# Optimization experiments

Hardware: AMD Instinct MI355X
Metric: run time of the kernel (lower is better)

The kernel has to match this reference:

```python
import jax, jax.numpy as jnp
import numpy as np

B, N, E, D, H, K = 64, 2048, 512, 256, 256, 5
I = E + D  # GRU input dim


def setup_inputs() -> dict:
    key = jax.random.key(0)
    ks = jax.random.split(key, 12)
    s = 0.05  # weight init scale
    enc_z = jax.random.normal(ks[0], (B, N, E), jnp.float32)
    dec_z = jax.random.normal(ks[1], (B, D), jnp.float32)
    h0 = jax.random.normal(ks[2], (1, B, H), jnp.float32)
    # GRU params (torch layout: gates ordered r, z, n)
    W_ih = jax.random.normal(ks[3], (3 * H, I), jnp.float32) * s
    W_hh = jax.random.normal(ks[4], (3 * H, H), jnp.float32) * s
    b_ih = jax.random.normal(ks[5], (3 * H,), jnp.float32) * s
    b_hh = jax.random.normal(ks[6], (3 * H,), jnp.float32) * s
    # K per-component MLPs: Linear(H,H) -> tanh -> Linear(H,3), stacked over K
    W1 = jax.random.normal(ks[7], (K, H, H), jnp.float32) * s
    b1 = jax.random.normal(ks[8], (K, H), jnp.float32) * s
    W2 = jax.random.normal(ks[9], (K, 3, H), jnp.float32) * s
    b2 = jax.random.normal(ks[10], (K, 3), jnp.float32) * s
    return {"enc_z": enc_z, "dec_z": dec_z, "h0": h0,
            "W_ih": W_ih, "W_hh": W_hh, "b_ih": b_ih, "b_hh": b_hh,
            "W1": W1, "b1": b1, "W2": W2, "b2": b2, "i": 0}


def reference(enc_z, dec_z, h0, W_ih, W_hh, b_ih, b_hh, W1, b1, W2, b2, i):
    # i == 0 -> reset: c = zeros, means = zeros, h = h0 (provided)
    Bt, Nt, Et = enc_z.shape
    Ht = h0.shape[-1]
    Kt = W1.shape[0]
    c0 = jnp.zeros((Bt, Et), enc_z.dtype)
    means = jnp.zeros((Bt, Kt), enc_z.dtype)
    # --- single-step GRU (torch semantics, gate order r,z,n) ---
    x = jnp.concatenate([dec_z, c0], axis=1)          # (B, I)
    h_prev = h0[0]                                    # (B, H)
    gi = x @ W_ih.T + b_ih                            # (B, 3H)
    gh = h_prev @ W_hh.T + b_hh                       # (B, 3H)
    r = jax.nn.sigmoid(gi[:, :Ht] + gh[:, :Ht])
    z = jax.nn.sigmoid(gi[:, Ht:2 * Ht] + gh[:, Ht:2 * Ht])
    n = jnp.tanh(gi[:, 2 * Ht:] + r * gh[:, 2 * Ht:])
    h_new = (1.0 - z) * n + z * h_prev                # (B, H)
    # --- K per-component MLPs, vectorized over K ---
    hid = jnp.tanh(jnp.einsum('khd,bd->bkh', W1, h_new) + b1)  # (B, K, H)
    params = jnp.einsum('kph,bkh->bkp', W2, hid) + b2           # (B, K, 3)
    # NOTE: the original code overwrites mean/scale each loop iteration, so
    # only the LAST component's mean/scale survive into the CDF loop.
    mean = means[:, Kt - 1] + jnp.exp(params[:, Kt - 1, 0])     # (B,)
    scale = jnp.exp(params[:, Kt - 1, 1])                       # (B,)
    weights = jax.nn.softmax(params[:, :, 2], axis=1)           # (B, K)
    # --- mixture-of-logistics CDF differences, vectorized over (B, N) ---
    # original _logistic: sigmoid(x - mean/scale)  (faithful to source, incl. its precedence)
    j = jnp.arange(Nt, dtype=enc_z.dtype)                       # (N,)
    arg = (mean / scale)[:, None]                               # (B, 1)
    f1 = jax.nn.sigmoid(j[None, :] + 0.5 - arg)                 # (B, N)
    f2 = jax.nn.sigmoid(j[None, :] - 0.5 - arg)                 # (B, N)
    # sum_k weights[:,k]*(f1-f2) with k-independent f1,f2 == weights.sum(1)*(f1-f2)
    a = weights.sum(axis=1, keepdims=True) * (f1 - f2)          # (B, N)
    c = jnp.einsum('bn,bne->be', a, enc_z)                      # (B, E)
    return (c[None], h_new[None])
```

## Files before the change

kernel.cpp:

```cpp
#include <hip/hip_runtime.h>
#include <hip/hip_bf16.h>
#include <cstdint>
#include <cstddef>

constexpr int B = 64, N = 2048, E = 512, D = 256, H = 256, K = 5, I = 768;

__device__ __forceinline__ float sg(float x) { return 1.0f / (1.0f + __expf(-x)); }

__device__ __forceinline__ void dot4(float4 v, const float* s, float& acc) {
  acc += v.x * s[0];
  acc += v.y * s[1];
  acc += v.z * s[2];
  acc += v.w * s[3];
}

__global__ __launch_bounds__(256) void fused(
    const float* __restrict__ enc, const float* __restrict__ dec,
    const float* __restrict__ h0,
    const float* __restrict__ Wih, const float* __restrict__ Whh,
    const float* __restrict__ bih, const float* __restrict__ bhh,
    const float* __restrict__ W1,  const float* __restrict__ b1,
    const float* __restrict__ W2,  const float* __restrict__ b2,
    float* __restrict__ out_c, float* __restrict__ out_h)
{
  __shared__ float xs[D], hs[H], hn[H], hid[K][H], pr[16];
  __shared__ float s_arg;
  const int b = blockIdx.x, t = threadIdx.x;
  xs[t] = dec[b * D + t];
  hs[t] = h0[b * H + t];
  __syncthreads();

  float gir = bih[t], giz = bih[H + t], gin = bih[2*H + t];
  float ghr = bhh[t], ghz = bhh[H + t], ghn = bhh[2*H + t];
  const float4* wr = reinterpret_cast<const float4*>(Wih + (size_t)t         * I);
  const float4* wz = reinterpret_cast<const float4*>(Wih + (size_t)(H + t)   * I);
  const float4* wn = reinterpret_cast<const float4*>(Wih + (size_t)(2*H + t) * I);
  const float4* ur = reinterpret_cast<const float4*>(Whh + (size_t)t         * H);
  const float4* uz = reinterpret_cast<const float4*>(Whh + (size_t)(H + t)   * H);
  const float4* un = reinterpret_cast<const float4*>(Whh + (size_t)(2*H + t) * H);
#pragma unroll 8
  for (int c = 0; c < 64; ++c) {
    dot4(wr[c], &xs[c*4], gir);
    dot4(wz[c], &xs[c*4], giz);
    dot4(wn[c], &xs[c*4], gin);
    dot4(ur[c], &hs[c*4], ghr);
    dot4(uz[c], &hs[c*4], ghz);
    dot4(un[c], &hs[c*4], ghn);
  }
  const float r = sg(gir + ghr);
  const float z = sg(giz + ghz);
  const float nn = tanhf(gin + r * ghn);
  const float hnew = (1.0f - z) * nn + z * hs[t];
  hn[t] = hnew;
  out_h[b * H + t] = hnew;
  __syncthreads();

#pragma unroll
  for (int k = 0; k < K; ++k) {
    float acc = b1[k * H + t];
    const float4* w = reinterpret_cast<const float4*>(W1 + ((size_t)k * H + t) * H);
#pragma unroll 8
    for (int c = 0; c < 64; ++c) dot4(w[c], &hn[c*4], acc);
    hid[k][t] = tanhf(acc);
  }
  __syncthreads();

  if (t < 240) {
    const int g = t >> 4, sub = t & 15;
    const int k = g / 3, p = g % 3;
    float s = 0.0f;
#pragma unroll
    for (int c = 0; c < 16; ++c) {
      const int h = sub + 16 * c;
      s += hid[k][h] * W2[(k * 3 + p) * H + h];
    }
    s += __shfl_xor(s, 8, 16);
    s += __shfl_xor(s, 4, 16);
    s += __shfl_xor(s, 2, 16);
    s += __shfl_xor(s, 1, 16);
    if (sub == 0) pr[g] = s + b2[k * 3 + p];
  }
  __syncthreads();

  if (t == 0) s_arg = __expf(pr[3 * (K - 1)] - pr[3 * (K - 1) + 1]);
  __syncthreads();

  const float arg = s_arg;
  const float lim = ceilf(arg) + 32.0f;
  int nmax = (lim < (float)N) ? (int)lim : N;
  if (nmax < 1) nmax = 1;

  const float2* src = reinterpret_cast<const float2*>(enc + (size_t)b * N * E) + t;
  float a0 = 0.0f, a1 = 0.0f;
#pragma unroll 4
  for (int n = 0; n < nmax; ++n) {
    const float fn = (float)n;
    const float an = sg(fn + 0.5f - arg) - sg(fn - 0.5f - arg);
    const float2 v = src[(size_t)n * (E / 2)];
    a0 += an * v.x;
    a1 += an * v.y;
  }
  out_c[b * E + 2 * t]     = a0;
  out_c[b * E + 2 * t + 1] = a1;
}

extern "C" void kernel_launch(void* const* d_in, const int* in_sizes, int n_in,
                              void* d_out, int out_size, void* d_ws, size_t ws_size,
                              hipStream_t stream) {
  const float* enc = (const float*)d_in[0];
  const float* dec = (const float*)d_in[1];
  const float* h0  = (const float*)d_in[2];
  const float* Wih = (const float*)d_in[3];
  const float* Whh = (const float*)d_in[4];
  const float* bih = (const float*)d_in[5];
  const float* bhh = (const float*)d_in[6];
  const float* W1  = (const float*)d_in[7];
  const float* b1  = (const float*)d_in[8];
  const float* W2  = (const float*)d_in[9];
  const float* b2  = (const float*)d_in[10];
  (void)in_sizes; (void)n_in; (void)out_size; (void)d_ws; (void)ws_size;

  float* out_c = (float*)d_out;
  float* out_h = out_c + (size_t)B * E;

  hipLaunchKernelGGL(fused, dim3(B), dim3(256), 0, stream,
                     enc, dec, h0, Wih, Whh, bih, bhh, W1, b1, W2, b2,
                     out_c, out_h);
}
```

Before: 404.9 us.

## Double block size and split GRU and MLP matvecs across thread halves

Launches 512 threads per batch block instead of 256. One half computes the input-gate matvec and the other the hidden-gate matvec, combining them through shared memory. The W1 matvec is also split by input halves with partial sums reduced in shared memory. The enc reduction now gives each thread one column instead of two. This shortens the per-thread serial dot-product chains in a kernel with only 64 blocks, at the cost of extra shared memory and syncs.

```diff
diff --git a/kernel.cpp b/kernel.cpp
--- a/kernel.cpp
+++ b/kernel.cpp
@@ -1,5 +1,4 @@
 #include <hip/hip_runtime.h>
-#include <hip/hip_bf16.h>
 #include <cstdint>
 #include <cstddef>
 
@@ -14,7 +13,7 @@
   acc += v.w * s[3];
 }
 
-__global__ __launch_bounds__(256) void fused(
+__global__ __launch_bounds__(512) void fused(
     const float* __restrict__ enc, const float* __restrict__ dec,
     const float* __restrict__ h0,
     const float* __restrict__ Wih, const float* __restrict__ Whh,
@@ -23,45 +22,58 @@
     const float* __restrict__ W2,  const float* __restrict__ b2,
     float* __restrict__ out_c, float* __restrict__ out_h)
 {
-  __shared__ float xs[D], hs[H], hn[H], hid[K][H], pr[16];
+  __shared__ float xs[D], hs[H], hn[H], ghs[3][H];
+  __shared__ float pl[K][H], pu[K][H], hid[K][H], pr[16];
   __shared__ float s_arg;
   const int b = blockIdx.x, t = threadIdx.x;
-  xs[t] = dec[b * D + t];
-  hs[t] = h0[b * H + t];
+  if (t < D) xs[t] = dec[b * D + t];
+  else       hs[t - D] = h0[b * H + (t - D)];
   __syncthreads();
 
-  float gir = bih[t], giz = bih[H + t], gin = bih[2*H + t];
-  float ghr = bhh[t], ghz = bhh[H + t], ghn = bhh[2*H + t];
-  const float4* wr = reinterpret_cast<const float4*>(Wih + (size_t)t         * I);
-  const float4* wz = reinterpret_cast<const float4*>(Wih + (size_t)(H + t)   * I);
-  const float4* wn = reinterpret_cast<const float4*>(Wih + (size_t)(2*H + t) * I);
-  const float4* ur = reinterpret_cast<const float4*>(Whh + (size_t)t         * H);
-  const float4* uz = reinterpret_cast<const float4*>(Whh + (size_t)(H + t)   * H);
-  const float4* un = reinterpret_cast<const float4*>(Whh + (size_t)(2*H + t) * H);
+  const bool lo = t < H;
+  const int  j  = t & (H - 1);
+  const float* Wb   = lo ? Wih : Whh;
+  const float* vec  = lo ? xs  : hs;
+  const float* bias = lo ? bih : bhh;
+  const size_t rs   = lo ? (size_t)I : (size_t)H;
+  float gr = bias[j], gz = bias[H + j], gn = bias[2 * H + j];
+  const float4* wr = reinterpret_cast<const float4*>(Wb + (size_t)j         * rs);
+  const float4* wz = reinterpret_cast<const float4*>(Wb + (size_t)(H + j)   * rs);
+  const float4* wn = reinterpret_cast<const float4*>(Wb + (size_t)(2*H + j) * rs);
 #pragma unroll 8
   for (int c = 0; c < 64; ++c) {
-    dot4(wr[c], &xs[c*4], gir);
-    dot4(wz[c], &xs[c*4], giz);
-    dot4(wn[c], &xs[c*4], gin);
-    dot4(ur[c], &hs[c*4], ghr);
-    dot4(uz[c], &hs[c*4], ghz);
-    dot4(un[c], &hs[c*4], ghn);
+    dot4(wr[c], &vec[c*4], gr);
+    dot4(wz[c], &vec[c*4], gz);
+    dot4(wn[c], &vec[c*4], gn);
   }
-  const float r = sg(gir + ghr);
-  const float z = sg(giz + ghz);
-  const float nn = tanhf(gin + r * ghn);
-  const float hnew = (1.0f - z) * nn + z * hs[t];
-  hn[t] = hnew;
-  out_h[b * H + t] = hnew;
+  if (!lo) { ghs[0][j] = gr; ghs[1][j] = gz; ghs[2][j] = gn; }
+  __syncthreads();
+  if (lo) {
+    const float r  = sg(gr + ghs[0][j]);
+    const float z  = sg(gz + ghs[1][j]);
+    const float nn = tanhf(gn + r * ghs[2][j]);
+    const float hnew = (1.0f - z) * nn + z * hs[j];
+    hn[j] = hnew;
+    out_h[b * H + j] = hnew;
+  }
   __syncthreads();
 
+  const float* hhalf = hn + (lo ? 0 : 128);
+  float (*pp)[H] = lo ? pl : pu;
 #pragma unroll
   for (int k = 0; k < K; ++k) {
-    float acc = b1[k * H + t];
-    const float4* w = reinterpret_cast<const float4*>(W1 + ((size_t)k * H + t) * H);
+    float acc = 0.0f;
+    const float4* w = reinterpret_cast<const float4*>(
+        W1 + ((size_t)k * H + j) * H + (lo ? 0 : 128));
 #pragma unroll 8
-    for (int c = 0; c < 64; ++c) dot4(w[c], &hn[c*4], acc);
-    hid[k][t] = tanhf(acc);
+    for (int c = 0; c < 32; ++c) dot4(w[c], &hhalf[c*4], acc);
+    pp[k][j] = acc;
+  }
+  __syncthreads();
+  if (lo) {
+#pragma unroll
+    for (int k = 0; k < K; ++k)
+      hid[k][j] = tanhf(pl[k][j] + pu[k][j] + b1[k * H + j]);
   }
   __syncthreads();
 
@@ -90,18 +102,15 @@
   int nmax = (lim < (float)N) ? (int)lim : N;
   if (nmax < 1) nmax = 1;
 
-  const float2* src = reinterpret_cast<const float2*>(enc + (size_t)b * N * E) + t;
-  float a0 = 0.0f, a1 = 0.0f;
+  const float* src = enc + (size_t)b * N * E + t;
+  float acc = 0.0f;
 #pragma unroll 4
   for (int n = 0; n < nmax; ++n) {
     const float fn = (float)n;
     const float an = sg(fn + 0.5f - arg) - sg(fn - 0.5f - arg);
-    const float2 v = src[(size_t)n * (E / 2)];
-    a0 += an * v.x;
-    a1 += an * v.y;
+    acc += an * src[(size_t)n * E];
   }
-  out_c[b * E + 2 * t]     = a0;
-  out_c[b * E + 2 * t + 1] = a1;
+  out_c[b * E + t] = acc;
 }
 
 extern "C" void kernel_launch(void* const* d_in, const int* in_sizes, int n_in,
@@ -123,7 +132,7 @@
   float* out_c = (float*)d_out;
   float* out_h = out_c + (size_t)B * E;
 
-  hipLaunchKernelGGL(fused, dim3(B), dim3(256), 0, stream,
+  hipLaunchKernelGGL(fused, dim3(B), dim3(512), 0, stream,
                      enc, dec, h0, Wih, Whh, bih, bhh, W1, b1, W2, b2,
                      out_c, out_h);
 }
```

After: 408.8 us. About the same (+1.0%).
